# Performance work log

Measured on AMD Instinct MI355X. Metric: run time of the kernel, lower is better.

## Reference

```python
import jax, jax.numpy as jnp
import numpy as np

B, N = 4, 2048
INPUT_DIM, KDIM, VDIM = 128, 128, 16
EMBED, V_EMBED, H = 128, 128, 8
HEAD_DIM = EMBED // H          # 16
V_HEAD_DIM = V_EMBED // H      # 16 (== VDIM, required by the torch view)
SCALING = HEAD_DIM ** -0.5


def setup_inputs() -> dict:
    key = jax.random.key(0)
    ks = jax.random.split(key, 12)
    inp = {
        "query": jax.random.normal(ks[0], (B, N, INPUT_DIM), dtype=jnp.float32),
        "key": jax.random.normal(ks[1], (B, N, KDIM), dtype=jnp.float32),
        "value": jax.random.normal(ks[2], (B, N, VDIM), dtype=jnp.float32),
        # nn.Linear weights are [out, in]; init.normal_ -> std normal
        "Wq": jax.random.normal(ks[3], (EMBED, INPUT_DIM), dtype=jnp.float32),
        "bq": jnp.zeros((EMBED,), dtype=jnp.float32),
        "Wk": jax.random.normal(ks[4], (EMBED, KDIM), dtype=jnp.float32),
        "bk": jnp.zeros((EMBED,), dtype=jnp.float32),
        "Wv": jax.random.normal(ks[5], (V_EMBED, VDIM), dtype=jnp.float32),
        "bv": jnp.zeros((V_EMBED,), dtype=jnp.float32),
        "Wo": jax.random.normal(ks[6], (V_EMBED // H, V_EMBED), dtype=jnp.float32),
        "bo": jnp.zeros((V_EMBED // H,), dtype=jnp.float32),
    }
    return inp


def reference(query, key, value, Wq, bq, Wk, bk, Wv, bv, Wo, bo):
    # projections
    q = (query @ Wq.T + bq) * SCALING                 # [B, N, EMBED]
    k = key @ Wk.T + bk                               # [B, N, EMBED]
    v = value @ Wv.T + bv                             # [B, N, V_EMBED]
    # split heads: [B, H, N, head_dim]
    q = q.reshape(B, N, H, HEAD_DIM).transpose(0, 2, 1, 3)
    k = k.reshape(B, N, H, HEAD_DIM).transpose(0, 2, 1, 3)
    v = v.reshape(B, N, H, V_HEAD_DIM).transpose(0, 2, 1, 3)
    # full NxN scores (naive attention, as in the source)
    scores = jnp.einsum("bhnd,bhmd->bhnm", q, k)      # [B, H, N, N]
    attn = jax.nn.softmax(scores, axis=-1)
    # dropout is identity in eval mode
    ctx = jnp.einsum("bhnm,bhme->bhne", attn, v)      # [B, H, N, V_HEAD_DIM]
    ctx = ctx.transpose(0, 2, 1, 3).reshape(B, N, V_EMBED)
    out = ctx @ Wo.T + bo                             # [B, N, V_EMBED // H]
    return out
```

## Files before the change

### kernel.cpp

```cpp
#include <hip/hip_runtime.h>
#include <hip/hip_bf16.h>
#include <math.h>

typedef unsigned short ushort_t;
typedef unsigned int uint_t;
typedef __bf16 bf16x8 __attribute__((ext_vector_type(8)));
typedef float f32x4 __attribute__((ext_vector_type(4)));

#define NSEQ 2048
#define BH   32
#define QSCALE 0.3606737602222409f

__device__ __forceinline__ float exp2_fast(float x) {
#if __has_builtin(__builtin_amdgcn_exp2f)
    return __builtin_amdgcn_exp2f(x);
#else
    return exp2f(x);
#endif
}

union U8 { ushort_t u[8]; bf16x8 v; uint4 q; uint_t w[4]; };
union F8 { float f[8]; float4 v4[2]; };

__device__ __forceinline__ uint_t pk2(float a, float b) {
    __hip_bfloat162 h2 = __float22bfloat162_rn(make_float2(a, b));
    union { __hip_bfloat162 h; uint_t u; } cv; cv.h = h2; return cv.u;
}

__device__ __forceinline__ void split8(const F8& x, U8& hi, U8& lo) {
#pragma unroll
    for (int p = 0; p < 4; ++p) {
        const float a = x.f[2*p], b = x.f[2*p+1];
        const uint_t hw = pk2(a, b);
        hi.w[p] = hw;
        const float ha = __uint_as_float(hw << 16);
        const float hb = __uint_as_float(hw & 0xFFFF0000u);
        lo.w[p] = pk2(a - ha, b - hb);
    }
}

__global__ __launch_bounds__(256) void wpack_kernel(
    const float* __restrict__ Wq, const float* __restrict__ Wk,
    ushort_t* __restrict__ wpk_hi, ushort_t* __restrict__ wpk_lo)
{
    const int idx  = blockIdx.x * 256 + threadIdx.x;
    const int lane = idx & 63;
    const int f    = (idx >> 6) & 3;
    const int ct   = (idx >> 8) & 7;
    const int mat  = idx >> 11;
    const float* W = mat ? Wk : Wq;
    const float* src = W + (size_t)(ct * 16 + (lane & 15)) * 128
                         + f * 32 + (lane >> 4) * 8;
    F8 x; x.v4[0] = *(const float4*)src; x.v4[1] = *(const float4*)(src + 4);
    U8 hi, lo;
    split8(x, hi, lo);
    const size_t dst = (size_t)mat * 16384 + ((size_t)(ct * 4 + f) * 64 + lane) * 8;
    *(uint4*)(wpk_hi + dst) = hi.q;
    *(uint4*)(wpk_lo + dst) = lo.q;
}

__global__ __launch_bounds__(256, 2) void proj_kernel(
    const float* __restrict__ query, const float* __restrict__ key,
    const float* __restrict__ value,
    const float* __restrict__ bq, const float* __restrict__ bk,
    const float* __restrict__ Wv, const float* __restrict__ bv,
    const ushort_t* __restrict__ wpk_hi, const ushort_t* __restrict__ wpk_lo,
    ushort_t* __restrict__ q_hi, ushort_t* __restrict__ q_lo,
    ushort_t* __restrict__ k_hi, ushort_t* __restrict__ k_lo,
    ushort_t* __restrict__ vt)
{
    const int t   = threadIdx.x;
    const int w   = t >> 6;
    const int l   = t & 63;
    const int n16 = l & 15;
    const int g   = l >> 4;
    const int rbase = blockIdx.x * 16;
    const int b = rbase >> 11;

    const int isK    = w >> 1;
    const int cthalf = (w & 1) * 4;

    const float* X = isK ? key : query;
    const float* xrow = X + (size_t)(rbase + n16) * 128 + g * 8;
    bf16x8 ah[4], al[4];
#pragma unroll
    for (int f = 0; f < 4; ++f) {
        F8 x;
        x.v4[0] = *(const float4*)(xrow + f * 32);
        x.v4[1] = *(const float4*)(xrow + f * 32 + 4);
        U8 hi, lo;
        split8(x, hi, lo);
        ah[f] = hi.v; al[f] = lo.v;
    }

    const float* bias = isK ? bk : bq;
    ushort_t* dhi = isK ? k_hi : q_hi;
    ushort_t* dlo = isK ? k_lo : q_lo;
    const float scale = isK ? 1.0f : QSCALE;
    const int nbase = (rbase & 2047) + g * 4;

#pragma unroll 1
    for (int ctl = 0; ctl < 4; ++ctl) {
        const int h = cthalf + ctl;
        bf16x8 bhf[4], blf[4];
#pragma unroll
        for (int f = 0; f < 4; ++f) {
            const size_t o = (size_t)isK * 16384
                           + ((size_t)(h * 4 + f) * 64 + l) * 8;
            bhf[f] = *(const bf16x8*)(wpk_hi + o);
            blf[f] = *(const bf16x8*)(wpk_lo + o);
        }
        const float bval = bias[h * 16 + n16];
        f32x4 acc = {bval, bval, bval, bval};
#pragma unroll
        for (int f = 0; f < 4; ++f) {
            acc = __builtin_amdgcn_mfma_f32_16x16x32_bf16(ah[f], bhf[f], acc, 0, 0, 0);
            acc = __builtin_amdgcn_mfma_f32_16x16x32_bf16(al[f], bhf[f], acc, 0, 0, 0);
            acc = __builtin_amdgcn_mfma_f32_16x16x32_bf16(ah[f], blf[f], acc, 0, 0, 0);
        }
        const size_t abase = ((size_t)(b * 8 + h) * NSEQ + nbase) * 16 + n16;
        const float a0 = acc[0]*scale, a1 = acc[1]*scale;
        const float a2 = acc[2]*scale, a3 = acc[3]*scale;
        const uint_t h01 = pk2(a0, a1), h23 = pk2(a2, a3);
        const uint_t l01 = pk2(a0 - __uint_as_float(h01 << 16),
                               a1 - __uint_as_float(h01 & 0xFFFF0000u));
        const uint_t l23 = pk2(a2 - __uint_as_float(h23 << 16),
                               a3 - __uint_as_float(h23 & 0xFFFF0000u));
        dhi[abase]      = (ushort_t)h01;
        dhi[abase + 16] = (ushort_t)(h01 >> 16);
        dhi[abase + 32] = (ushort_t)h23;
        dhi[abase + 48] = (ushort_t)(h23 >> 16);
        dlo[abase]      = (ushort_t)l01;
        dlo[abase + 16] = (ushort_t)(l01 >> 16);
        dlo[abase + 32] = (ushort_t)l23;
        dlo[abase + 48] = (ushort_t)(l23 >> 16);
    }

    const int e  = t & 127;
    const int rh = t >> 7;
    const int r0 = rbase + rh * 8;
    const float4* Wv4 = (const float4*)(Wv + (size_t)e * 16);
    const float4 wv0 = Wv4[0], wv1 = Wv4[1], wv2 = Wv4[2], wv3 = Wv4[3];
    const float bvv = bv[e];
    F8 af;
#pragma unroll
    for (int r = 0; r < 8; ++r) {
        const float4* xv4 = (const float4*)(value + (size_t)(r0 + r) * 16);
        const float4 x0 = xv4[0], x1 = xv4[1], x2 = xv4[2], x3 = xv4[3];
        float a = bvv;
        a += wv0.x*x0.x + wv0.y*x0.y + wv0.z*x0.z + wv0.w*x0.w;
        a += wv1.x*x1.x + wv1.y*x1.y + wv1.z*x1.z + wv1.w*x1.w;
        a += wv2.x*x2.x + wv2.y*x2.y + wv2.z*x2.z + wv2.w*x2.w;
        a += wv3.x*x3.x + wv3.y*x3.y + wv3.z*x3.z + wv3.w*x3.w;
        af.f[r] = a;
    }
    U8 vpk;
#pragma unroll
    for (int p = 0; p < 4; ++p) vpk.w[p] = pk2(af.f[2*p], af.f[2*p+1]);
    const int hv = e >> 4, dd = e & 15;
    *(uint4*)(vt + ((size_t)(b * 8 + hv) * 16 + dd) * NSEQ + (r0 & 2047)) = vpk.q;
}

__global__ __launch_bounds__(256, 2) void maxk_kernel(
    const ushort_t* __restrict__ q_hi,
    const ushort_t* __restrict__ k_hi, const ushort_t* __restrict__ k_lo,
    float* __restrict__ m_arr)
{
    const int t    = threadIdx.x;
    const int wave = t >> 6;
    const int l    = t & 63;
    const int col  = l & 15;
    const int g    = l >> 4;

    const int bh = blockIdx.y;
    const int qb = blockIdx.x * 64 + wave * 16;

    const size_t qoff = ((size_t)(bh * NSEQ + qb + col)) * 16 + (g & 1) * 8;
    const bf16x8 bq1 = *(const bf16x8*)(q_hi + qoff);

    const ushort_t* ksel = (g < 2) ? k_hi : k_lo;
    const ushort_t* aptr = ksel + ((size_t)(bh * NSEQ + col)) * 16 + (g & 1) * 8;

    float mrun = -INFINITY;
    const f32x4 z = {0.f, 0.f, 0.f, 0.f};
#pragma unroll 2
    for (int kb = 0; kb < 64; ++kb) {
        const bf16x8 a1 = *(const bf16x8*)(aptr + (size_t)kb * 512);
        const bf16x8 a2 = *(const bf16x8*)(aptr + (size_t)kb * 512 + 256);
        const f32x4 st1 = __builtin_amdgcn_mfma_f32_16x16x32_bf16(a1, bq1, z, 0, 0, 0);
        const f32x4 st2 = __builtin_amdgcn_mfma_f32_16x16x32_bf16(a2, bq1, z, 0, 0, 0);
        mrun = fmaxf(mrun, fmaxf(fmaxf(st1[0], st1[1]), fmaxf(st1[2], st1[3])));
        mrun = fmaxf(mrun, fmaxf(fmaxf(st2[0], st2[1]), fmaxf(st2[2], st2[3])));
    }
    mrun = fmaxf(mrun, __shfl_xor(mrun, 16));
    mrun = fmaxf(mrun, __shfl_xor(mrun, 32));
    if (l < 16) m_arr[bh * NSEQ + qb + col] = mrun;
}

__global__ __launch_bounds__(256, 2) void attn_kernel(
    const ushort_t* __restrict__ q_hi, const ushort_t* __restrict__ q_lo,
    const ushort_t* __restrict__ k_hi, const ushort_t* __restrict__ k_lo,
    const ushort_t* __restrict__ vt, const float* __restrict__ m_arr,
    float* __restrict__ ctx)
{
    const int t    = threadIdx.x;
    const int wave = t >> 6;
    const int l    = t & 63;
    const int col  = l & 15;
    const int g    = l >> 4;

    const int bh = blockIdx.y;
    const int qb = blockIdx.x * 64 + wave * 16;

    __shared__ __align__(16) ushort_t lds_p[4][16 * 40];
    ushort_t* pbuf = lds_p[wave];

    U8 Uz, Uo;
#pragma unroll
    for (int i = 0; i < 8; ++i) { Uz.u[i] = 0; Uo.u[i] = 0x3F80; }
    const bf16x8 zf = Uz.v, ones = Uo.v;

    const size_t qoff = ((size_t)(bh * NSEQ + qb + col)) * 16 + (g & 1) * 8;
    const bf16x8 bq1 = *(const bf16x8*)(q_hi + qoff);
    bf16x8 bq2 = *(const bf16x8*)(q_lo + qoff);
    bq2 = (g < 2) ? bq2 : zf;

    const float mcol = m_arr[bh * NSEQ + qb + col];
    const f32x4 zin = {-mcol, -mcol, -mcol, -mcol};

    const ushort_t* ksel = (g < 2) ? k_hi : k_lo;
    const ushort_t* aptr = ksel + ((size_t)(bh * NSEQ + col)) * 16 + (g & 1) * 8;
    const ushort_t* vptr = vt + ((size_t)(bh * 16 + col)) * NSEQ + g * 8;

    f32x4 o    = {0.f, 0.f, 0.f, 0.f};
    f32x4 lacc = {0.f, 0.f, 0.f, 0.f};

    bf16x8 a1 = *(const bf16x8*)(aptr);
    bf16x8 a2 = *(const bf16x8*)(aptr + 256);
    bf16x8 av = *(const bf16x8*)(vptr);

    for (int kb = 0; kb < 64; ++kb) {
        const int kn = (kb + 1) & 63;
        bf16x8 na1 = *(const bf16x8*)(aptr + (size_t)kn * 512);
        bf16x8 na2 = *(const bf16x8*)(aptr + (size_t)kn * 512 + 256);
        bf16x8 nav = *(const bf16x8*)(vptr + (size_t)kn * 32);

        f32x4 st1 = __builtin_amdgcn_mfma_f32_16x16x32_bf16(a1, bq2, zin, 0, 0, 0);
        st1       = __builtin_amdgcn_mfma_f32_16x16x32_bf16(a1, bq1, st1, 0, 0, 0);
        f32x4 st2 = __builtin_amdgcn_mfma_f32_16x16x32_bf16(a2, bq2, zin, 0, 0, 0);
        st2       = __builtin_amdgcn_mfma_f32_16x16x32_bf16(a2, bq1, st2, 0, 0, 0);

        const float p0 = exp2_fast(st1[0]);
        const float p1 = exp2_fast(st1[1]);
        const float p2 = exp2_fast(st1[2]);
        const float p3 = exp2_fast(st1[3]);
        const float p4 = exp2_fast(st2[0]);
        const float p5 = exp2_fast(st2[1]);
        const float p6 = exp2_fast(st2[2]);
        const float p7 = exp2_fast(st2[3]);

        uint2 w1; w1.x = pk2(p0, p1); w1.y = pk2(p2, p3);
        uint2 w2; w2.x = pk2(p4, p5); w2.y = pk2(p6, p7);
        *(uint2*)(pbuf + col * 40 + 4 * g)      = w1;
        *(uint2*)(pbuf + col * 40 + 16 + 4 * g) = w2;
        const bf16x8 bp = *(const bf16x8*)(pbuf + col * 40 + 8 * g);

        o    = __builtin_amdgcn_mfma_f32_16x16x32_bf16(av,   bp, o,    0, 0, 0);
        lacc = __builtin_amdgcn_mfma_f32_16x16x32_bf16(ones, bp, lacc, 0, 0, 0);

        a1 = na1; a2 = na2; av = nav;
    }

    const float linv = 1.0f / lacc[0];
    f32x4 res;
    res[0] = o[0] * linv; res[1] = o[1] * linv;
    res[2] = o[2] * linv; res[3] = o[3] * linv;
    *(f32x4*)(ctx + ((size_t)(bh * NSEQ + qb + col)) * 16 + 4 * g) = res;
}

__global__ __launch_bounds__(256) void outproj_kernel(
    const float* __restrict__ ctxws, const float* __restrict__ Wo,
    const float* __restrict__ bo, float* __restrict__ out)
{
    __shared__ float wo_s[16 * 132];
    const int t = threadIdx.x;
    for (int i = t; i < 2048; i += 256) {
        const int j = i >> 7, e2 = i & 127;
        wo_s[j * 132 + e2] = Wo[i];
    }
    __syncthreads();

    const int rl = t >> 4, j = t & 15;
    const int row = blockIdx.x * 16 + rl;
    const int b = row >> 11, n = row & 2047;
    float acc = bo[j];
#pragma unroll
    for (int h = 0; h < 8; ++h) {
        const float4* cp4 = (const float4*)(ctxws + (((size_t)(b*8 + h) * NSEQ) + n) * 16);
#pragma unroll
        for (int d4 = 0; d4 < 4; ++d4) {
            const float4 cc = cp4[d4];
            const float* wp = &wo_s[j * 132 + h * 16 + d4 * 4];
            acc += cc.x*wp[0] + cc.y*wp[1] + cc.z*wp[2] + cc.w*wp[3];
        }
    }
    out[(size_t)row * 16 + j] = acc;
}

extern "C" void kernel_launch(void* const* d_in, const int* in_sizes, int n_in,
                              void* d_out, int out_size, void* d_ws, size_t ws_size,
                              hipStream_t stream)
{
    const float* query = (const float*)d_in[0];
    const float* key_  = (const float*)d_in[1];
    const float* value = (const float*)d_in[2];
    const float* Wq = (const float*)d_in[3];
    const float* bq = (const float*)d_in[4];
    const float* Wk = (const float*)d_in[5];
    const float* bk = (const float*)d_in[6];
    const float* Wv = (const float*)d_in[7];
    const float* bv = (const float*)d_in[8];
    const float* Wo = (const float*)d_in[9];
    const float* bo = (const float*)d_in[10];
    float* out = (float*)d_out;

    ushort_t* q_hi = (ushort_t*)d_ws;
    ushort_t* q_lo = q_hi + (1u << 20);
    ushort_t* k_hi = q_hi + (2u << 20);
    ushort_t* k_lo = q_hi + (3u << 20);
    ushort_t* vt   = q_hi + (4u << 20);
    float*    ctx  = (float*)((char*)d_ws + (10u << 20));
    ushort_t* wpk_hi = (ushort_t*)((char*)d_ws + (14u << 20));
    ushort_t* wpk_lo = wpk_hi + 32768;
    float*    m_arr  = (float*)((char*)d_ws + (14u << 20) + (1u << 18));

    wpack_kernel<<<dim3(16), dim3(256), 0, stream>>>(Wq, Wk, wpk_hi, wpk_lo);
    proj_kernel<<<dim3(512), dim3(256), 0, stream>>>(
        query, key_, value, bq, bk, Wv, bv, wpk_hi, wpk_lo,
        q_hi, q_lo, k_hi, k_lo, vt);
    maxk_kernel<<<dim3(32, 32), dim3(256), 0, stream>>>(q_hi, k_hi, k_lo, m_arr);
    attn_kernel<<<dim3(32, 32), dim3(256), 0, stream>>>(
        q_hi, q_lo, k_hi, k_lo, vt, m_arr, ctx);
    outproj_kernel<<<dim3(512), dim3(256), 0, stream>>>(ctx, Wo, bo, out);
}
```

Measured before the change: 158.5 us.

## Fuse max pass into attention, split keys across waves, use fp16 PV and MFMA outproj

The separate max-score kernel is folded into the attention kernel. Each block now splits the key range between wave pairs, which combine their maxima and partial outputs through LDS. The PV product switches from an LDS round-trip of bf16 probabilities to fp16 16x16x16 MFMAs fed directly from registers, with V stored as fp16. The context is written as bf16 in row-major [B,N,128] layout, and the output projection uses bf16 hi/lo-split MFMAs on Wo that is prepacked in the weight-pack kernel. The aim is to remove a kernel launch and the LDS traffic and raise occupancy, at the cost of extra bf16 rounding on the context and fp16 round-toward-zero on the probabilities.

```diff
diff --git a/kernel.cpp b/kernel.cpp
--- a/kernel.cpp
+++ b/kernel.cpp
@@ -6,9 +6,10 @@
 typedef unsigned int uint_t;
 typedef __bf16 bf16x8 __attribute__((ext_vector_type(8)));
 typedef float f32x4 __attribute__((ext_vector_type(4)));
+typedef __fp16 fp16v2 __attribute__((ext_vector_type(2)));
+typedef _Float16 f16x4 __attribute__((ext_vector_type(4)));
 
 #define NSEQ 2048
-#define BH   32
 #define QSCALE 0.3606737602222409f
 
 __device__ __forceinline__ float exp2_fast(float x) {
@@ -21,6 +22,8 @@
 
 union U8 { ushort_t u[8]; bf16x8 v; uint4 q; uint_t w[4]; };
 union F8 { float f[8]; float4 v4[2]; };
+union H4 { fp16v2 h2[2]; f16x4 v; uint_t w[2]; };
+union HV { fp16v2 h2[4]; uint4 q; };
 
 __device__ __forceinline__ uint_t pk2(float a, float b) {
     __hip_bfloat162 h2 = __float22bfloat162_rn(make_float2(a, b));
@@ -41,22 +44,38 @@
 
 __global__ __launch_bounds__(256) void wpack_kernel(
     const float* __restrict__ Wq, const float* __restrict__ Wk,
-    ushort_t* __restrict__ wpk_hi, ushort_t* __restrict__ wpk_lo)
-{
-    const int idx  = blockIdx.x * 256 + threadIdx.x;
-    const int lane = idx & 63;
-    const int f    = (idx >> 6) & 3;
-    const int ct   = (idx >> 8) & 7;
-    const int mat  = idx >> 11;
-    const float* W = mat ? Wk : Wq;
-    const float* src = W + (size_t)(ct * 16 + (lane & 15)) * 128
-                         + f * 32 + (lane >> 4) * 8;
-    F8 x; x.v4[0] = *(const float4*)src; x.v4[1] = *(const float4*)(src + 4);
-    U8 hi, lo;
-    split8(x, hi, lo);
-    const size_t dst = (size_t)mat * 16384 + ((size_t)(ct * 4 + f) * 64 + lane) * 8;
-    *(uint4*)(wpk_hi + dst) = hi.q;
-    *(uint4*)(wpk_lo + dst) = lo.q;
+    const float* __restrict__ Wo,
+    ushort_t* __restrict__ wpk_hi, ushort_t* __restrict__ wpk_lo,
+    ushort_t* __restrict__ wo_hi, ushort_t* __restrict__ wo_lo)
+{
+    const int idx = blockIdx.x * 256 + threadIdx.x;
+    if (idx < 4096) {
+        const int lane = idx & 63;
+        const int f    = (idx >> 6) & 3;
+        const int ct   = (idx >> 8) & 7;
+        const int mat  = idx >> 11;
+        const float* W = mat ? Wk : Wq;
+        const float* src = W + (size_t)(ct * 16 + (lane & 15)) * 128
+                             + f * 32 + (lane >> 4) * 8;
+        F8 x; x.v4[0] = *(const float4*)src; x.v4[1] = *(const float4*)(src + 4);
+        U8 hi, lo;
+        split8(x, hi, lo);
+        const size_t dst = (size_t)mat * 16384 + ((size_t)(ct * 4 + f) * 64 + lane) * 8;
+        *(uint4*)(wpk_hi + dst) = hi.q;
+        *(uint4*)(wpk_lo + dst) = lo.q;
+    } else if (idx < 4352) {
+        const int i2   = idx - 4096;
+        const int lane = i2 & 63;
+        const int f    = i2 >> 6;
+        const float* src = Wo + (size_t)(lane & 15) * 128
+                              + f * 32 + (lane >> 4) * 8;
+        F8 x; x.v4[0] = *(const float4*)src; x.v4[1] = *(const float4*)(src + 4);
+        U8 hi, lo;
+        split8(x, hi, lo);
+        const size_t dst = ((size_t)f * 64 + lane) * 8;
+        *(uint4*)(wo_hi + dst) = hi.q;
+        *(uint4*)(wo_lo + dst) = lo.q;
+    }
 }
 
 __global__ __launch_bounds__(256, 2) void proj_kernel(
@@ -154,157 +173,146 @@
         a += wv3.x*x3.x + wv3.y*x3.y + wv3.z*x3.z + wv3.w*x3.w;
         af.f[r] = a;
     }
-    U8 vpk;
-#pragma unroll
-    for (int p = 0; p < 4; ++p) vpk.w[p] = pk2(af.f[2*p], af.f[2*p+1]);
+    HV vpk;
+#pragma unroll
+    for (int p = 0; p < 4; ++p)
+        vpk.h2[p] = __builtin_amdgcn_cvt_pkrtz(af.f[2*p], af.f[2*p+1]);
     const int hv = e >> 4, dd = e & 15;
     *(uint4*)(vt + ((size_t)(b * 8 + hv) * 16 + dd) * NSEQ + (r0 & 2047)) = vpk.q;
 }
 
-__global__ __launch_bounds__(256, 2) void maxk_kernel(
-    const ushort_t* __restrict__ q_hi,
+__global__ __launch_bounds__(256, 6) void attn_kernel(
+    const ushort_t* __restrict__ q_hi, const ushort_t* __restrict__ q_lo,
     const ushort_t* __restrict__ k_hi, const ushort_t* __restrict__ k_lo,
-    float* __restrict__ m_arr)
+    const ushort_t* __restrict__ vt, ushort_t* __restrict__ ctxb)
 {
     const int t    = threadIdx.x;
-    const int wave = t >> 6;
+    const int w    = t >> 6;
     const int l    = t & 63;
     const int col  = l & 15;
     const int g    = l >> 4;
+    const int qsub = w & 1;
+    const int kh   = w >> 1;
 
     const int bh = blockIdx.y;
-    const int qb = blockIdx.x * 64 + wave * 16;
-
-    const size_t qoff = ((size_t)(bh * NSEQ + qb + col)) * 16 + (g & 1) * 8;
-    const bf16x8 bq1 = *(const bf16x8*)(q_hi + qoff);
-
-    const ushort_t* ksel = (g < 2) ? k_hi : k_lo;
-    const ushort_t* aptr = ksel + ((size_t)(bh * NSEQ + col)) * 16 + (g & 1) * 8;
-
-    float mrun = -INFINITY;
-    const f32x4 z = {0.f, 0.f, 0.f, 0.f};
-#pragma unroll 2
-    for (int kb = 0; kb < 64; ++kb) {
-        const bf16x8 a1 = *(const bf16x8*)(aptr + (size_t)kb * 512);
-        const bf16x8 a2 = *(const bf16x8*)(aptr + (size_t)kb * 512 + 256);
-        const f32x4 st1 = __builtin_amdgcn_mfma_f32_16x16x32_bf16(a1, bq1, z, 0, 0, 0);
-        const f32x4 st2 = __builtin_amdgcn_mfma_f32_16x16x32_bf16(a2, bq1, z, 0, 0, 0);
-        mrun = fmaxf(mrun, fmaxf(fmaxf(st1[0], st1[1]), fmaxf(st1[2], st1[3])));
-        mrun = fmaxf(mrun, fmaxf(fmaxf(st2[0], st2[1]), fmaxf(st2[2], st2[3])));
-    }
-    mrun = fmaxf(mrun, __shfl_xor(mrun, 16));
-    mrun = fmaxf(mrun, __shfl_xor(mrun, 32));
-    if (l < 16) m_arr[bh * NSEQ + qb + col] = mrun;
-}
-
-__global__ __launch_bounds__(256, 2) void attn_kernel(
-    const ushort_t* __restrict__ q_hi, const ushort_t* __restrict__ q_lo,
-    const ushort_t* __restrict__ k_hi, const ushort_t* __restrict__ k_lo,
-    const ushort_t* __restrict__ vt, const float* __restrict__ m_arr,
-    float* __restrict__ ctx)
-{
-    const int t    = threadIdx.x;
-    const int wave = t >> 6;
-    const int l    = t & 63;
-    const int col  = l & 15;
-    const int g    = l >> 4;
-
-    const int bh = blockIdx.y;
-    const int qb = blockIdx.x * 64 + wave * 16;
-
-    __shared__ __align__(16) ushort_t lds_p[4][16 * 40];
-    ushort_t* pbuf = lds_p[wave];
-
-    U8 Uz, Uo;
-#pragma unroll
-    for (int i = 0; i < 8; ++i) { Uz.u[i] = 0; Uo.u[i] = 0x3F80; }
-    const bf16x8 zf = Uz.v, ones = Uo.v;
+    const int qb = blockIdx.x * 32 + qsub * 16;
+
+    __shared__ float lds_m[64];
+    __shared__ __align__(16) float lds_o[4][16][16];
+    __shared__ float lds_l[4][16];
+
+    U8 Uz;
+#pragma unroll
+    for (int i = 0; i < 8; ++i) Uz.u[i] = 0;
+    const bf16x8 zf = Uz.v;
 
     const size_t qoff = ((size_t)(bh * NSEQ + qb + col)) * 16 + (g & 1) * 8;
     const bf16x8 bq1 = *(const bf16x8*)(q_hi + qoff);
     bf16x8 bq2 = *(const bf16x8*)(q_lo + qoff);
     bq2 = (g < 2) ? bq2 : zf;
 
-    const float mcol = m_arr[bh * NSEQ + qb + col];
-    const f32x4 zin = {-mcol, -mcol, -mcol, -mcol};
-
     const ushort_t* ksel = (g < 2) ? k_hi : k_lo;
-    const ushort_t* aptr = ksel + ((size_t)(bh * NSEQ + col)) * 16 + (g & 1) * 8;
-    const ushort_t* vptr = vt + ((size_t)(bh * 16 + col)) * NSEQ + g * 8;
+    const ushort_t* aptr = ksel + ((size_t)bh * NSEQ + col) * 16 + (g & 1) * 8
+                         + (size_t)kh * 1024 * 16;
+    const ushort_t* vp = vt + ((size_t)bh * 16 + col) * NSEQ + kh * 1024;
+
+    float mrun = -INFINITY;
+    const f32x4 z = {0.f, 0.f, 0.f, 0.f};
+#pragma unroll 2
+    for (int kb = 0; kb < 32; ++kb) {
+        const bf16x8 a1 = *(const bf16x8*)(aptr + (size_t)kb * 512);
+        const bf16x8 a2 = *(const bf16x8*)(aptr + (size_t)kb * 512 + 256);
+        const f32x4 s1 = __builtin_amdgcn_mfma_f32_16x16x32_bf16(a1, bq1, z, 0, 0, 0);
+        const f32x4 s2 = __builtin_amdgcn_mfma_f32_16x16x32_bf16(a2, bq1, z, 0, 0, 0);
+        mrun = fmaxf(mrun, fmaxf(fmaxf(s1[0], s1[1]), fmaxf(s1[2], s1[3])));
+        mrun = fmaxf(mrun, fmaxf(fmaxf(s2[0], s2[1]), fmaxf(s2[2], s2[3])));
+    }
+    mrun = fmaxf(mrun, __shfl_xor(mrun, 16));
+    mrun = fmaxf(mrun, __shfl_xor(mrun, 32));
+    if (l < 16) lds_m[w * 16 + col] = mrun;
+    __syncthreads();
+    const float mfin = fmaxf(mrun, lds_m[(w ^ 2) * 16 + col]);
+    const f32x4 zin = {-mfin, -mfin, -mfin, -mfin};
 
     f32x4 o    = {0.f, 0.f, 0.f, 0.f};
     f32x4 lacc = {0.f, 0.f, 0.f, 0.f};
+    const f16x4 onesh = {(_Float16)1.f, (_Float16)1.f, (_Float16)1.f, (_Float16)1.f};
 
     bf16x8 a1 = *(const bf16x8*)(aptr);
     bf16x8 a2 = *(const bf16x8*)(aptr + 256);
-    bf16x8 av = *(const bf16x8*)(vptr);
-
-    for (int kb = 0; kb < 64; ++kb) {
-        const int kn = (kb + 1) & 63;
+    f16x4 av1 = *(const f16x4*)(vp + g * 4);
+    f16x4 av2 = *(const f16x4*)(vp + 16 + g * 4);
+
+    for (int kb = 0; kb < 32; ++kb) {
+        const int kn = (kb + 1) & 31;
         bf16x8 na1 = *(const bf16x8*)(aptr + (size_t)kn * 512);
         bf16x8 na2 = *(const bf16x8*)(aptr + (size_t)kn * 512 + 256);
-        bf16x8 nav = *(const bf16x8*)(vptr + (size_t)kn * 32);
+        f16x4 nav1 = *(const f16x4*)(vp + kn * 32 + g * 4);
+        f16x4 nav2 = *(const f16x4*)(vp + kn * 32 + 16 + g * 4);
 
         f32x4 st1 = __builtin_amdgcn_mfma_f32_16x16x32_bf16(a1, bq2, zin, 0, 0, 0);
         st1       = __builtin_amdgcn_mfma_f32_16x16x32_bf16(a1, bq1, st1, 0, 0, 0);
         f32x4 st2 = __builtin_amdgcn_mfma_f32_16x16x32_bf16(a2, bq2, zin, 0, 0, 0);
         st2       = __builtin_amdgcn_mfma_f32_16x16x32_bf16(a2, bq1, st2, 0, 0, 0);
 
-        const float p0 = exp2_fast(st1[0]);
-        const float p1 = exp2_fast(st1[1]);
-        const float p2 = exp2_fast(st1[2]);
-        const float p3 = exp2_fast(st1[3]);
-        const float p4 = exp2_fast(st2[0]);
-        const float p5 = exp2_fast(st2[1]);
-        const float p6 = exp2_fast(st2[2]);
-        const float p7 = exp2_fast(st2[3]);
-
-        uint2 w1; w1.x = pk2(p0, p1); w1.y = pk2(p2, p3);
-        uint2 w2; w2.x = pk2(p4, p5); w2.y = pk2(p6, p7);
-        *(uint2*)(pbuf + col * 40 + 4 * g)      = w1;
-        *(uint2*)(pbuf + col * 40 + 16 + 4 * g) = w2;
-        const bf16x8 bp = *(const bf16x8*)(pbuf + col * 40 + 8 * g);
-
-        o    = __builtin_amdgcn_mfma_f32_16x16x32_bf16(av,   bp, o,    0, 0, 0);
-        lacc = __builtin_amdgcn_mfma_f32_16x16x32_bf16(ones, bp, lacc, 0, 0, 0);
-
-        a1 = na1; a2 = na2; av = nav;
-    }
-
-    const float linv = 1.0f / lacc[0];
-    f32x4 res;
-    res[0] = o[0] * linv; res[1] = o[1] * linv;
-    res[2] = o[2] * linv; res[3] = o[3] * linv;
-    *(f32x4*)(ctx + ((size_t)(bh * NSEQ + qb + col)) * 16 + 4 * g) = res;
+        H4 b1u, b2u;
+        b1u.h2[0] = __builtin_amdgcn_cvt_pkrtz(exp2_fast(st1[0]), exp2_fast(st1[1]));
+        b1u.h2[1] = __builtin_amdgcn_cvt_pkrtz(exp2_fast(st1[2]), exp2_fast(st1[3]));
+        b2u.h2[0] = __builtin_amdgcn_cvt_pkrtz(exp2_fast(st2[0]), exp2_fast(st2[1]));
+        b2u.h2[1] = __builtin_amdgcn_cvt_pkrtz(exp2_fast(st2[2]), exp2_fast(st2[3]));
+
+        o    = __builtin_amdgcn_mfma_f32_16x16x16f16(av1,   b1u.v, o,    0, 0, 0);
+        lacc = __builtin_amdgcn_mfma_f32_16x16x16f16(onesh, b1u.v, lacc, 0, 0, 0);
+        o    = __builtin_amdgcn_mfma_f32_16x16x16f16(av2,   b2u.v, o,    0, 0, 0);
+        lacc = __builtin_amdgcn_mfma_f32_16x16x16f16(onesh, b2u.v, lacc, 0, 0, 0);
+
+        a1 = na1; a2 = na2; av1 = nav1; av2 = nav2;
+    }
+
+    *(f32x4*)&lds_o[w][col][4 * g] = o;
+    if (l < 16) lds_l[w][col] = lacc[0];
+    __syncthreads();
+    if (w < 2) {
+        const f32x4 oA = *(const f32x4*)&lds_o[w][col][4 * g];
+        const f32x4 oB = *(const f32x4*)&lds_o[w + 2][col][4 * g];
+        const float li = 1.0f / (lds_l[w][col] + lds_l[w + 2][col]);
+        const float r0 = (oA[0] + oB[0]) * li;
+        const float r1 = (oA[1] + oB[1]) * li;
+        const float r2 = (oA[2] + oB[2]) * li;
+        const float r3 = (oA[3] + oB[3]) * li;
+        const int b = bh >> 3, h = bh & 7;
+        uint2 pkd; pkd.x = pk2(r0, r1); pkd.y = pk2(r2, r3);
+        *(uint2*)(ctxb + ((size_t)(b * NSEQ + qb + col)) * 128 + h * 16 + 4 * g) = pkd;
+    }
 }
 
 __global__ __launch_bounds__(256) void outproj_kernel(
-    const float* __restrict__ ctxws, const float* __restrict__ Wo,
+    const ushort_t* __restrict__ ctxb,
+    const ushort_t* __restrict__ wo_hi, const ushort_t* __restrict__ wo_lo,
     const float* __restrict__ bo, float* __restrict__ out)
 {
-    __shared__ float wo_s[16 * 132];
-    const int t = threadIdx.x;
-    for (int i = t; i < 2048; i += 256) {
-        const int j = i >> 7, e2 = i & 127;
-        wo_s[j * 132 + e2] = Wo[i];
-    }
-    __syncthreads();
-
-    const int rl = t >> 4, j = t & 15;
-    const int row = blockIdx.x * 16 + rl;
-    const int b = row >> 11, n = row & 2047;
-    float acc = bo[j];
-#pragma unroll
-    for (int h = 0; h < 8; ++h) {
-        const float4* cp4 = (const float4*)(ctxws + (((size_t)(b*8 + h) * NSEQ) + n) * 16);
-#pragma unroll
-        for (int d4 = 0; d4 < 4; ++d4) {
-            const float4 cc = cp4[d4];
-            const float* wp = &wo_s[j * 132 + h * 16 + d4 * 4];
-            acc += cc.x*wp[0] + cc.y*wp[1] + cc.z*wp[2] + cc.w*wp[3];
-        }
-    }
-    out[(size_t)row * 16 + j] = acc;
+    const int t   = threadIdx.x;
+    const int w   = t >> 6;
+    const int l   = t & 63;
+    const int col = l & 15;
+    const int g   = l >> 4;
+    const int row0 = blockIdx.x * 64 + w * 16;
+
+    const float bval = bo[col];
+    f32x4 acc = {bval, bval, bval, bval};
+    const ushort_t* ar = ctxb + (size_t)(row0 + col) * 128 + g * 8;
+#pragma unroll
+    for (int f = 0; f < 4; ++f) {
+        const bf16x8 a = *(const bf16x8*)(ar + f * 32);
+        const size_t o = ((size_t)f * 64 + l) * 8;
+        const bf16x8 bh_ = *(const bf16x8*)(wo_hi + o);
+        const bf16x8 bl_ = *(const bf16x8*)(wo_lo + o);
+        acc = __builtin_amdgcn_mfma_f32_16x16x32_bf16(a, bh_, acc, 0, 0, 0);
+        acc = __builtin_amdgcn_mfma_f32_16x16x32_bf16(a, bl_, acc, 0, 0, 0);
+    }
+#pragma unroll
+    for (int r = 0; r < 4; ++r)
+        out[(size_t)(row0 + 4 * g + r) * 16 + col] = acc[r];
 }
 
 extern "C" void kernel_launch(void* const* d_in, const int* in_sizes, int n_in,
@@ -324,22 +332,25 @@
     const float* bo = (const float*)d_in[10];
     float* out = (float*)d_out;
 
-    ushort_t* q_hi = (ushort_t*)d_ws;
-    ushort_t* q_lo = q_hi + (1u << 20);
-    ushort_t* k_hi = q_hi + (2u << 20);
-    ushort_t* k_lo = q_hi + (3u << 20);
-    ushort_t* vt   = q_hi + (4u << 20);
-    float*    ctx  = (float*)((char*)d_ws + (10u << 20));
-    ushort_t* wpk_hi = (ushort_t*)((char*)d_ws + (14u << 20));
+    ushort_t* base = (ushort_t*)d_ws;
+    ushort_t* q_hi = base;
+    ushort_t* q_lo = base + (1u << 20);
+    ushort_t* k_hi = base + (2u << 20);
+    ushort_t* k_lo = base + (3u << 20);
+    ushort_t* vt   = base + (4u << 20);
+    ushort_t* ctxb = base + (5u << 20);
+    ushort_t* wpk_hi = base + (6u << 20);
     ushort_t* wpk_lo = wpk_hi + 32768;
-    float*    m_arr  = (float*)((char*)d_ws + (14u << 20) + (1u << 18));
-
-    wpack_kernel<<<dim3(16), dim3(256), 0, stream>>>(Wq, Wk, wpk_hi, wpk_lo);
+    ushort_t* wo_hi  = wpk_hi + 65536;
+    ushort_t* wo_lo  = wo_hi + 2048;
+
+    wpack_kernel<<<dim3(17), dim3(256), 0, stream>>>(
+        Wq, Wk, Wo, wpk_hi, wpk_lo, wo_hi, wo_lo);
     proj_kernel<<<dim3(512), dim3(256), 0, stream>>>(
         query, key_, value, bq, bk, Wv, bv, wpk_hi, wpk_lo,
         q_hi, q_lo, k_hi, k_lo, vt);
-    maxk_kernel<<<dim3(32, 32), dim3(256), 0, stream>>>(q_hi, k_hi, k_lo, m_arr);
-    attn_kernel<<<dim3(32, 32), dim3(256), 0, stream>>>(
-        q_hi, q_lo, k_hi, k_lo, vt, m_arr, ctx);
-    outproj_kernel<<<dim3(512), dim3(256), 0, stream>>>(ctx, Wo, bo, out);
-}
+    attn_kernel<<<dim3(64, 32), dim3(256), 0, stream>>>(
+        q_hi, q_lo, k_hi, k_lo, vt, ctxb);
+    outproj_kernel<<<dim3(128), dim3(256), 0, stream>>>(
+        ctxb, wo_hi, wo_lo, bo, out);
+}
```

Result: slower. 183.7 us (+15.9%).
